# Performance work log

Hardware: AMD Instinct MI355X
Metric: run time of the kernel (lower is better)

Reference implementation:

```python
import jax, jax.numpy as jnp
import numpy as np

N = 1024  # codeword length (power of 2)
K = 512   # info bits
BATCH = 65536
NB_STAGES = int(np.log2(N))  # 10


def _gen_indices(n):
    """Stage-wise gather indices; index n points at a sentinel zero column."""
    nb_stages = int(np.log2(n))
    ind_gather = np.full((nb_stages, n + 1), n, dtype=np.int32)
    for s in range(nb_stages):
        ind_range = np.arange(n // 2)
        ind_dest = ind_range * 2 - np.mod(ind_range, 2 ** s)
        ind_gather[s, ind_dest] = ind_dest + 2 ** s
    return ind_gather


def setup_inputs() -> dict:
    key = jax.random.key(0)
    # binary information bits, float32 as in the original layer
    u = jax.random.randint(key, (BATCH, K), 0, 2).astype(jnp.float32)
    frozen_pos = np.arange(N - K)
    info_pos = jnp.asarray(np.setdiff1d(np.arange(N), frozen_pos), dtype=jnp.int32)  # [K]
    ind_gather = jnp.asarray(_gen_indices(N))  # [NB_STAGES, N+1]
    return {"u": u, "info_pos": info_pos, "ind_gather": ind_gather}


def reference(u, info_pos, ind_gather) -> jnp.ndarray:
    b = u.shape[0]
    # scatter info bits into codeword positions; frozen positions stay 0
    c = jnp.zeros((b, N), u.dtype).at[:, info_pos].set(u)
    # append sentinel zero column at index N (gather target for pass-through lanes)
    x = jnp.concatenate([c, jnp.zeros((b, 1), u.dtype)], axis=1)  # [b, N+1]
    # log2(N)-stage butterfly: XOR == add mod 2 for binary values
    for s in range(NB_STAGES):
        x = jnp.mod(x + x[:, ind_gather[s]], 2.0)
    return x[:, :N]
```

## Files before the change

### kernel.cpp

```cpp
#include <hip/hip_runtime.h>


#define PN     1024
#define PK     512
#define PBATCH 65536
#define ROUNDS 16

typedef float vf4 __attribute__((ext_vector_type(4)));

__global__ __launch_bounds__(256) void build_inv_kernel(
    const int* __restrict__ info_pos, int* __restrict__ inv)
{
    const int tid = threadIdx.x;
    #pragma unroll
    for (int i = tid; i < PN; i += 256) inv[i] = -1;
    __syncthreads();
    #pragma unroll
    for (int k = tid; k < PK; k += 256) inv[info_pos[k]] = k;
}

__device__ __forceinline__ void encode_row(
    const float* __restrict__ u,
    const int*   __restrict__ inv,
    float*       __restrict__ srow,
    vf4*         __restrict__ out4,
    int lane, unsigned row)
{
    const float4* u4 = (const float4*)(u + (size_t)row * PK);
    const float4 a0 = u4[lane];
    const float4 a1 = u4[64 + lane];
    float4* s4 = (float4*)srow;
    s4[lane]      = a0;
    s4[64 + lane] = a1;

    const int l31 = lane & 31;

    unsigned int word = 0;
    #pragma unroll
    for (int c = 0; c < ROUNDS; ++c) {
        const int   iv  = inv[c * 64 + lane];
        const float v   = srow[iv & (PK - 1)];
        const bool  bit = (iv >= 0) && (v != 0.0f);
        const unsigned long long m = __ballot(bit);
        const unsigned int sel =
            (l31 & 1) ? (unsigned int)(m >> 32) : (unsigned int)m;
        if ((l31 >> 1) == c) word = sel;
    }

    word ^= (word >> 1)  & 0x55555555u;
    word ^= (word >> 2)  & 0x33333333u;
    word ^= (word >> 4)  & 0x0F0F0F0Fu;
    word ^= (word >> 8)  & 0x00FF00FFu;
    word ^= (word >> 16) & 0x0000FFFFu;

    #pragma unroll
    for (int off = 1; off <= 16; off <<= 1) {
        const unsigned int partner =
            (unsigned int)__shfl_xor((int)word, off, 64);
        if ((l31 & off) == 0) word ^= partner;
    }

    const unsigned base = row * (PN / 4);
    #pragma unroll
    for (int j = 0; j < 4; ++j) {
        const int f   = j * 64 + lane;
        const int src = f >> 3;
        const unsigned int b   = (unsigned int)__shfl((int)word, src, 64);
        const unsigned int nib = (b >> ((f & 7) * 4)) & 0xFu;
        vf4 v;
        v.x = (nib & 1u) ? 1.0f : 0.0f;
        v.y = (nib & 2u) ? 1.0f : 0.0f;
        v.z = (nib & 4u) ? 1.0f : 0.0f;
        v.w = (nib & 8u) ? 1.0f : 0.0f;
        __builtin_nontemporal_store(v, out4 + base + f);
    }
}

__global__ __launch_bounds__(256) void polar_encode_kernel(
    const float* __restrict__ u,
    const int*   __restrict__ ginv,
    vf4*         __restrict__ out4)
{
    __shared__ float su[4][PK];
    const int tid  = threadIdx.x;
    const int lane = tid & 63;
    const int wave = tid >> 6;
    const unsigned row = blockIdx.x * 4u + wave;
    encode_row(u, ginv, su[wave], out4, lane, row);
}

__global__ __launch_bounds__(256) void polar_fused_kernel(
    const float* __restrict__ u,
    const int*   __restrict__ info_pos,
    vf4*         __restrict__ out4)
{
    __shared__ int   inv[PN];
    __shared__ float su[4][PK];
    const int tid = threadIdx.x;
    #pragma unroll
    for (int i = tid; i < PN; i += 256) inv[i] = -1;
    __syncthreads();
    #pragma unroll
    for (int k = tid; k < PK; k += 256) inv[info_pos[k]] = k;
    __syncthreads();

    const int lane = tid & 63;
    const int wave = tid >> 6;
    const unsigned row = blockIdx.x * 4u + wave;
    encode_row(u, inv, su[wave], out4, lane, row);
}

extern "C" void kernel_launch(void* const* d_in, const int* in_sizes, int n_in,
                              void* d_out, int out_size, void* d_ws, size_t ws_size,
                              hipStream_t stream) {
    const float* u        = (const float*)d_in[0];
    const int*   info_pos = (const int*)d_in[1];
    vf4* out4 = (vf4*)d_out;

    if (ws_size >= (size_t)PN * 4) {
        int* inv = (int*)d_ws;
        build_inv_kernel<<<1, 256, 0, stream>>>(info_pos, inv);
        polar_encode_kernel<<<PBATCH / 4, 256, 0, stream>>>(u, inv, out4);
    } else {
        polar_fused_kernel<<<PBATCH / 4, 256, 0, stream>>>(u, info_pos, out4);
    }
}
```

Baseline: 355.8 us.

## Add fast path for contiguous upper-half info positions and fuse launches

```diff
diff --git a/kernel.cpp b/kernel.cpp
--- a/kernel.cpp
+++ b/kernel.cpp
@@ -4,40 +4,86 @@
 #define PN     1024
 #define PK     512
 #define PBATCH 65536
-#define ROUNDS 16
 
 typedef float vf4 __attribute__((ext_vector_type(4)));
 
-__global__ __launch_bounds__(256) void build_inv_kernel(
-    const int* __restrict__ info_pos, int* __restrict__ inv)
+__global__ __launch_bounds__(256) void polar_encode_kernel(
+    const float* __restrict__ u,
+    const int*   __restrict__ info_pos,
+    vf4*         __restrict__ out4)
 {
-    const int tid = threadIdx.x;
+    __shared__ int   inv[PN];
+    __shared__ float su[4][PK];
+
+    const int tid  = threadIdx.x;
+    const int lane = tid & 63;
+    const int wave = tid >> 6;
+    const unsigned row  = blockIdx.x * 4u + wave;
+    const unsigned base = row * (PN / 4);
+
+    const bool fast = (info_pos[0] == PK) && (info_pos[PK - 1] == PN - 1);
+
+    if (fast) {
+        const float4* u4 = (const float4*)(u + (size_t)row * PK);
+        const float4 a = u4[2 * lane];
+        const float4 b = u4[2 * lane + 1];
+        unsigned int byte =
+            ((unsigned)a.x)        | ((unsigned)a.y << 1) |
+            ((unsigned)a.z << 2)   | ((unsigned)a.w << 3) |
+            ((unsigned)b.x << 4)   | ((unsigned)b.y << 5) |
+            ((unsigned)b.z << 6)   | ((unsigned)b.w << 7);
+
+        byte ^= (byte >> 1) & 0x55u;
+        byte ^= (byte >> 2) & 0x33u;
+        byte ^= (byte >> 4) & 0x0Fu;
+        #pragma unroll
+        for (int off = 1; off <= 32; off <<= 1) {
+            const unsigned int p =
+                (unsigned int)__shfl_xor((int)byte, off, 64);
+            if ((lane & off) == 0) byte ^= p;
+        }
+
+        const unsigned int bEven =
+            (unsigned int)__shfl((int)byte, lane >> 1, 64);
+        const unsigned int bOdd =
+            (unsigned int)__shfl((int)byte, 32 + (lane >> 1), 64);
+        const unsigned int sh   = (lane & 1) * 4;
+        const unsigned int nibE = (bEven >> sh) & 0xFu;
+        const unsigned int nibO = (bOdd  >> sh) & 0xFu;
+
+        #pragma unroll
+        for (int j = 0; j < 4; ++j) {
+            const unsigned int nib = (j & 1) ? nibO : nibE;
+            vf4 v;
+            v.x = (nib & 1u) ? 1.0f : 0.0f;
+            v.y = (nib & 2u) ? 1.0f : 0.0f;
+            v.z = (nib & 4u) ? 1.0f : 0.0f;
+            v.w = (nib & 8u) ? 1.0f : 0.0f;
+            __builtin_nontemporal_store(v, out4 + base + j * 64 + lane);
+        }
+        return;
+    }
+
     #pragma unroll
     for (int i = tid; i < PN; i += 256) inv[i] = -1;
     __syncthreads();
     #pragma unroll
     for (int k = tid; k < PK; k += 256) inv[info_pos[k]] = k;
-}
+    __syncthreads();
 
-__device__ __forceinline__ void encode_row(
-    const float* __restrict__ u,
-    const int*   __restrict__ inv,
-    float*       __restrict__ srow,
-    vf4*         __restrict__ out4,
-    int lane, unsigned row)
-{
-    const float4* u4 = (const float4*)(u + (size_t)row * PK);
-    const float4 a0 = u4[lane];
-    const float4 a1 = u4[64 + lane];
-    float4* s4 = (float4*)srow;
-    s4[lane]      = a0;
-    s4[64 + lane] = a1;
-
+    float* srow = su[wave];
+    {
+        const float4* u4 = (const float4*)(u + (size_t)row * PK);
+        const float4 a0 = u4[lane];
+        const float4 a1 = u4[64 + lane];
+        float4* s4 = (float4*)srow;
+        s4[lane]      = a0;
+        s4[64 + lane] = a1;
+    }
     const int l31 = lane & 31;
-
     unsigned int word = 0;
     #pragma unroll
-    for (int c = 0; c < ROUNDS; ++c) {
+    for (int c = 0; c < PN / 64; ++c) {
         const int   iv  = inv[c * 64 + lane];
         const float v   = srow[iv & (PK - 1)];
         const bool  bit = (iv >= 0) && (v != 0.0f);
@@ -46,21 +92,17 @@
             (l31 & 1) ? (unsigned int)(m >> 32) : (unsigned int)m;
         if ((l31 >> 1) == c) word = sel;
     }
-
     word ^= (word >> 1)  & 0x55555555u;
     word ^= (word >> 2)  & 0x33333333u;
     word ^= (word >> 4)  & 0x0F0F0F0Fu;
     word ^= (word >> 8)  & 0x00FF00FFu;
     word ^= (word >> 16) & 0x0000FFFFu;
-
     #pragma unroll
     for (int off = 1; off <= 16; off <<= 1) {
         const unsigned int partner =
             (unsigned int)__shfl_xor((int)word, off, 64);
         if ((l31 & off) == 0) word ^= partner;
     }
-
-    const unsigned base = row * (PN / 4);
     #pragma unroll
     for (int j = 0; j < 4; ++j) {
         const int f   = j * 64 + lane;
@@ -76,40 +118,6 @@
     }
 }
 
-__global__ __launch_bounds__(256) void polar_encode_kernel(
-    const float* __restrict__ u,
-    const int*   __restrict__ ginv,
-    vf4*         __restrict__ out4)
-{
-    __shared__ float su[4][PK];
-    const int tid  = threadIdx.x;
-    const int lane = tid & 63;
-    const int wave = tid >> 6;
-    const unsigned row = blockIdx.x * 4u + wave;
-    encode_row(u, ginv, su[wave], out4, lane, row);
-}
-
-__global__ __launch_bounds__(256) void polar_fused_kernel(
-    const float* __restrict__ u,
-    const int*   __restrict__ info_pos,
-    vf4*         __restrict__ out4)
-{
-    __shared__ int   inv[PN];
-    __shared__ float su[4][PK];
-    const int tid = threadIdx.x;
-    #pragma unroll
-    for (int i = tid; i < PN; i += 256) inv[i] = -1;
-    __syncthreads();
-    #pragma unroll
-    for (int k = tid; k < PK; k += 256) inv[info_pos[k]] = k;
-    __syncthreads();
-
-    const int lane = tid & 63;
-    const int wave = tid >> 6;
-    const unsigned row = blockIdx.x * 4u + wave;
-    encode_row(u, inv, su[wave], out4, lane, row);
-}
-
 extern "C" void kernel_launch(void* const* d_in, const int* in_sizes, int n_in,
                               void* d_out, int out_size, void* d_ws, size_t ws_size,
                               hipStream_t stream) {
@@ -117,11 +125,5 @@
     const int*   info_pos = (const int*)d_in[1];
     vf4* out4 = (vf4*)d_out;
 
-    if (ws_size >= (size_t)PN * 4) {
-        int* inv = (int*)d_ws;
-        build_inv_kernel<<<1, 256, 0, stream>>>(info_pos, inv);
-        polar_encode_kernel<<<PBATCH / 4, 256, 0, stream>>>(u, inv, out4);
-    } else {
-        polar_fused_kernel<<<PBATCH / 4, 256, 0, stream>>>(u, info_pos, out4);
-    }
+    polar_encode_kernel<<<PBATCH / 4, 256, 0, stream>>>(u, info_pos, out4);
 }
```

After: 361.7 us. No clear change (+1.6%).
